# Optimization experiments

Measured on AMD Instinct MI355X. Metric: run time of the kernel, lower is better.

Reference implementation:

```python
import jax, jax.numpy as jnp
import numpy as np

N, E = 50000, 800000
IN, HID, OUT, H = 128, 32, 32, 4
NEG_SLOPE = 0.2
EPS = 1e-5


def layernorm(x, g, b):
    mu = x.mean(-1, keepdims=True)
    var = ((x - mu) ** 2).mean(-1, keepdims=True)
    return (x - mu) * jax.lax.rsqrt(var + EPS) * g + b


def gat_conv(x, src, dst, W, a_s, a_d, bias, heads, ch, concat):
    n = x.shape[0]
    h = (x @ W).reshape(n, heads, ch)               # [N,H,C]
    alpha_s = (h * a_s).sum(-1)                     # [N,H]
    alpha_d = (h * a_d).sum(-1)                     # [N,H]
    e = jax.nn.leaky_relu(alpha_s[src] + alpha_d[dst], NEG_SLOPE)  # [E,H]
    m = jax.ops.segment_max(e, dst, num_segments=n)
    m = jnp.where(jnp.isfinite(m), m, 0.0)
    ex = jnp.exp(e - m[dst])
    denom = jax.ops.segment_sum(ex, dst, num_segments=n)
    alpha = ex / (denom[dst] + 1e-16)               # [E,H]
    msg = h[src] * alpha[:, :, None]                # [E,H,C]
    out = jax.ops.segment_sum(msg, dst, num_segments=n)  # [N,H,C]
    out = out.reshape(n, heads * ch) if concat else out.mean(axis=1)
    return out + bias


def setup_inputs() -> dict:
    key = jax.random.key(0)
    ks = jax.random.split(key, 24)
    HC = HID * H
    s = 0.05
    inp = {
        "x": jax.random.normal(ks[0], (N, IN), jnp.float32),
        "edge_index": jax.random.randint(ks[1], (2, E), 0, N),
        "W1": jax.random.normal(ks[2], (IN, HC), jnp.float32) * s,
        "as1": jax.random.normal(ks[3], (H, HID), jnp.float32) * s,
        "ad1": jax.random.normal(ks[4], (H, HID), jnp.float32) * s,
        "b1": jnp.zeros((HC,), jnp.float32),
        "g1": jnp.ones((HC,), jnp.float32),
        "be1": jnp.zeros((HC,), jnp.float32),
        "W2": jax.random.normal(ks[5], (HC, HC), jnp.float32) * s,
        "as2": jax.random.normal(ks[6], (H, HID), jnp.float32) * s,
        "ad2": jax.random.normal(ks[7], (H, HID), jnp.float32) * s,
        "b2": jnp.zeros((HC,), jnp.float32),
        "g2": jnp.ones((HC,), jnp.float32),
        "be2": jnp.zeros((HC,), jnp.float32),
        "W3": jax.random.normal(ks[8], (HC, OUT * H), jnp.float32) * s,
        "as3": jax.random.normal(ks[9], (H, OUT), jnp.float32) * s,
        "ad3": jax.random.normal(ks[10], (H, OUT), jnp.float32) * s,
        "b3": jnp.zeros((OUT,), jnp.float32),
        "Wsk": jax.random.normal(ks[11], (IN, HC), jnp.float32) * s,
        "bsk": jnp.zeros((HC,), jnp.float32),
    }
    return inp


def reference(x, edge_index, W1, as1, ad1, b1, g1, be1, W2, as2, ad2, b2, g2, be2, W3, as3, ad3, b3, Wsk, bsk):
    n = x.shape[0]
    loops = jnp.arange(n, dtype=edge_index.dtype)
    src = jnp.concatenate([edge_index[0], loops])
    dst = jnp.concatenate([edge_index[1], loops])
    h = gat_conv(x, src, dst, W1, as1, ad1, b1, H, HID, True)
    h = jax.nn.elu(h)
    h = layernorm(h, g1, be1)
    h = h + (x @ Wsk + bsk)  # residual (dropout is identity in eval)
    h = gat_conv(h, src, dst, W2, as2, ad2, b2, H, HID, True)
    h = jax.nn.elu(h)
    h = layernorm(h, g2, be2)
    h = gat_conv(h, src, dst, W3, as3, ad3, b3, H, OUT, False)
    return h
```

## Files before the change

kernel.cpp:

```cpp
#include <hip/hip_runtime.h>
#include <hip/hip_bf16.h>

typedef __attribute__((ext_vector_type(8))) short short8;
typedef __attribute__((ext_vector_type(4))) float f32x4;
using bf16 = __hip_bfloat16;

#define NEG_SLOPE 0.2f
#define LN_EPS 1e-5f

__device__ __forceinline__ unsigned short f2bfu(float v) {
    bf16 t = __float2bfloat16(v);
    unsigned short s;
    __builtin_memcpy(&s, &t, 2);
    return s;
}
__device__ __forceinline__ short f2bf(float v) {
    bf16 t = __float2bfloat16(v);
    short s;
    __builtin_memcpy(&s, &t, 2);
    return s;
}
__device__ __forceinline__ unsigned packbf(float a, float b) {
    return (unsigned)f2bfu(a) | ((unsigned)f2bfu(b) << 16);
}
__device__ __forceinline__ float bflo(unsigned u) { return __uint_as_float(u << 16); }
__device__ __forceinline__ float bfhi(unsigned u) { return __uint_as_float(u & 0xffff0000u); }
__device__ __forceinline__ float bf1(unsigned short u) { return __uint_as_float(((unsigned)u) << 16); }

__global__ void detect_k(const void* __restrict__ x, int* flag,
                         int* bucketCur, int CAP) {
    int lane = threadIdx.x;
    for (int i = lane; i < 512; i += 64) bucketCur[i] = i * CAP;
    const unsigned short* u = (const unsigned short*)x;
    float m = 0.f;
    for (int i = lane; i < 8192; i += 64) {
        float v = fabsf(bf1(u[i]));
        if (!(v == v)) v = 1e30f;
        m = fmaxf(m, v);
    }
    for (int d = 1; d < 64; d <<= 1) m = fmaxf(m, __shfl_xor(m, d));
    if (lane == 0) flag[0] = (m > 1e4f) ? 1 : 0;
}

struct Ptr4 { const void* p[4]; };
struct Ptr14 { const void* p[14]; };
struct Ptr3 { const void* p[3]; };
struct Ptr6 { const void* p[6]; };
__global__ void stage_k(Ptr4 Ws, bf16* __restrict__ WT,
                        Ptr14 ptrs, bf16* __restrict__ sv,
                        Ptr3 Wv, Ptr6 av, bf16* __restrict__ vaT,
                        const int* __restrict__ flag) {
    int b = blockIdx.x;
    int f = flag[0];
    if (b < 256) {
        int gid = b * 256 + threadIdx.x;
        int m = gid >> 14;
        int idx = gid & 16383;
        int i = idx >> 7, j = idx & 127;
        const void* W = Ws.p[m];
        float v = f ? ((const float*)W)[idx]
                    : __bfloat162float(((const bf16*)W)[idx]);
        WT[m * 16384 + j * 128 + i] = __float2bfloat16(v);
    } else if (b == 256) {
        for (int k = threadIdx.x; k < 14 * 128; k += 256) {
            int t = k >> 7, i = k & 127;
            int n = (t == 12) ? 32 : 128;
            if (i < n) {
                const void* s = ptrs.p[t];
                float v = f ? ((const float*)s)[i]
                            : __bfloat162float(((const bf16*)s)[i]);
                sv[k] = __float2bfloat16(v);
            }
        }
    } else {
        int gid = (b - 257) * 256 + threadIdx.x;
        int l = gid >> 11;
        if (l >= 3) return;
        int c = (gid >> 7) & 15, k = gid & 127;
        float acc = 0.f;
        if (c < 8) {
            int hd = c & 3;
            const void* W = Wv.p[l];
            const void* a = av.p[l * 2 + (c >> 2)];
            for (int j = 0; j < 32; ++j) {
                float wv = f ? ((const float*)W)[k * 128 + hd * 32 + j]
                             : __bfloat162float(((const bf16*)W)[k * 128 + hd * 32 + j]);
                float avv = f ? ((const float*)a)[hd * 32 + j]
                              : __bfloat162float(((const bf16*)a)[hd * 32 + j]);
                acc += wv * avv;
            }
        }
        vaT[gid] = __float2bfloat16(acc);
    }
}

#define SCAT_EPB 2048
__global__ __launch_bounds__(256) void bscatter_k(const int* __restrict__ src,
                                                  const int* __restrict__ dst,
                                                  int* bucketCur,
                                                  int* __restrict__ ebuf,
                                                  int E, int NB, int CAP) {
    __shared__ int lcnt[512], lbase[512];
    int t = threadIdx.x;
    int e0 = blockIdx.x * SCAT_EPB;
    int cnt = E - e0;
    if (cnt > SCAT_EPB) cnt = SCAT_EPB;
    for (int i = t; i < NB; i += 256) lcnt[i] = 0;
    __syncthreads();
    for (int i = t; i < cnt; i += 256)
        atomicAdd(&lcnt[dst[e0 + i] >> 7], 1);
    __syncthreads();
    for (int i = t; i < NB; i += 256) {
        int c = lcnt[i];
        lbase[i] = c ? atomicAdd(&bucketCur[i], c) : 0;
        lcnt[i] = 0;
    }
    __syncthreads();
    for (int i = t; i < cnt; i += 256) {
        int d = dst[e0 + i];
        int b = d >> 7;
        int pos = lbase[b] + atomicAdd(&lcnt[b], 1);
        if (pos < (b + 1) * CAP)
            ebuf[pos] = ((d & 127) << 16) | src[e0 + i];
    }
}

__global__ __launch_bounds__(256) void build_k(const int* __restrict__ ebuf,
                                               const int* __restrict__ bucketCur,
                                               int* __restrict__ rowSE,
                                               int* __restrict__ colSrc,
                                               int N, int CAP) {
    int b = blockIdx.x, t = threadIdx.x;
    int base = b * CAP;
    int cnt = bucketCur[b] - base;
    if (cnt > CAP) cnt = CAP;
    __shared__ int nodeCnt[128], nodeCur[128], ws2[2];
    if (t < 128) nodeCnt[t] = 0;
    __syncthreads();
    for (int i = t; i < cnt; i += 256)
        atomicAdd(&nodeCnt[ebuf[base + i] >> 16], 1);
    __syncthreads();
    int v = 0, incl = 0;
    if (t < 128) {
        v = nodeCnt[t];
        incl = v;
        for (int d = 1; d < 64; d <<= 1) {
            int u = __shfl_up(incl, d);
            if ((t & 63) >= d) incl += u;
        }
        if ((t & 63) == 63) ws2[t >> 6] = incl;
    }
    __syncthreads();
    if (t < 128) {
        int excl = incl - v + ((t >= 64) ? ws2[0] : 0);
        int node = b * 128 + t;
        if (node < N) {
            rowSE[node * 2] = base + excl;
            rowSE[node * 2 + 1] = base + excl + v;
        }
        nodeCur[t] = excl;
    }
    __syncthreads();
    for (int i = t; i < cnt; i += 256) {
        int p = ebuf[base + i];
        int pos = base + atomicAdd(&nodeCur[p >> 16], 1);
        colSrc[pos] = (p & 0xffff) << 8;
    }
    int capz = CAP + ((b == (int)gridDim.x - 1) ? 32 : 0);
    for (int i = cnt + t; i < capz; i += 256)
        colSrc[base + i] = 0;
}

template <int DUAL>
__global__ __launch_bounds__(256) void gemm_k(const void* __restrict__ A,
                                              const bf16* __restrict__ WT,
                                              bf16* __restrict__ out0,
                                              bf16* __restrict__ out1,
                                              const bf16* __restrict__ bias1,
                                              const bf16* __restrict__ vaT,
                                              float* __restrict__ asN,
                                              float* __restrict__ adN,
                                              int N, const int* __restrict__ flag) {
    int wave = threadIdx.x >> 6, lane = threadIdx.x & 63;
    int lm = lane & 15, lk = lane >> 4;
    const short* Ws = (const short*)WT;
    const short* Vs = (const short*)vaT;
    bool f32m = flag && flag[0];

    short8 bw0[2][4], bw1[DUAL ? 2 : 1][DUAL ? 4 : 1];
#pragma unroll
    for (int ct = 0; ct < 2; ++ct) {
        int c = (wave * 2 + ct) * 16 + lm;
#pragma unroll
        for (int kk = 0; kk < 4; ++kk)
            bw0[ct][kk] = *(const short8*)(Ws + (size_t)c * 128 + kk * 32 + lk * 8);
    }
    if (DUAL) {
#pragma unroll
        for (int ct = 0; ct < 2; ++ct) {
            int c = (wave * 2 + ct) * 16 + lm;
#pragma unroll
            for (int kk = 0; kk < 4; ++kk)
                bw1[ct][kk] = *(const short8*)(Ws + 16384 + (size_t)c * 128 + kk * 32 + lk * 8);
        }
    }
    short8 va8[4];
    if (wave == 0) {
#pragma unroll
        for (int kk = 0; kk < 4; ++kk)
            va8[kk] = *(const short8*)(Vs + (size_t)lm * 128 + kk * 32 + lk * 8);
    }
    float bv[2][4];
    if (DUAL) {
#pragma unroll
        for (int ct = 0; ct < 2; ++ct) {
            int c0 = (wave * 2 + ct) * 16 + lk * 4;
#pragma unroll
            for (int i = 0; i < 4; ++i)
                bv[ct][i] = __bfloat162float(bias1[c0 + i]);
        }
    }

    int stride = gridDim.x * 32;
    for (int rowBase = blockIdx.x * 32; rowBase < N; rowBase += stride) {
        short8 af[2][4];
#pragma unroll
        for (int rt = 0; rt < 2; ++rt) {
            int r = rowBase + rt * 16 + lm;
            if (r >= N) r = N - 1;
            if (f32m) {
#pragma unroll
                for (int kk = 0; kk < 4; ++kk) {
                    const float* Af = (const float*)A + (size_t)r * 128 + kk * 32 + lk * 8;
                    float4 q0 = *(const float4*)(Af);
                    float4 q1 = *(const float4*)(Af + 4);
                    short8 v;
                    v[0] = f2bf(q0.x); v[1] = f2bf(q0.y); v[2] = f2bf(q0.z); v[3] = f2bf(q0.w);
                    v[4] = f2bf(q1.x); v[5] = f2bf(q1.y); v[6] = f2bf(q1.z); v[7] = f2bf(q1.w);
                    af[rt][kk] = v;
                }
            } else {
#pragma unroll
                for (int kk = 0; kk < 4; ++kk)
                    af[rt][kk] = *(const short8*)((const short*)A + (size_t)r * 128 + kk * 32 + lk * 8);
            }
        }

        f32x4 acc0[2][2];
        f32x4 acc1[DUAL ? 2 : 1][DUAL ? 2 : 1];
#pragma unroll
        for (int ct = 0; ct < 2; ++ct)
#pragma unroll
            for (int rt = 0; rt < 2; ++rt) acc0[ct][rt] = (f32x4){0.f, 0.f, 0.f, 0.f};
        if (DUAL) {
#pragma unroll
            for (int ct = 0; ct < 2; ++ct)
#pragma unroll
                for (int rt = 0; rt < 2; ++rt) acc1[ct][rt] = (f32x4){0.f, 0.f, 0.f, 0.f};
        }

#pragma unroll
        for (int rt = 0; rt < 2; ++rt) {
#pragma unroll
            for (int kk = 0; kk < 4; ++kk) {
                acc0[0][rt] = __builtin_amdgcn_mfma_f32_16x16x32_bf16(bw0[0][kk], af[rt][kk], acc0[0][rt], 0, 0, 0);
                acc0[1][rt] = __builtin_amdgcn_mfma_f32_16x16x32_bf16(bw0[1][kk], af[rt][kk], acc0[1][rt], 0, 0, 0);
                if (DUAL) {
                    acc1[0][rt] = __builtin_amdgcn_mfma_f32_16x16x32_bf16(bw1[0][kk], af[rt][kk], acc1[0][rt], 0, 0, 0);
                    acc1[1][rt] = __builtin_amdgcn_mfma_f32_16x16x32_bf16(bw1[1][kk], af[rt][kk], acc1[1][rt], 0, 0, 0);
                }
            }
        }

#pragma unroll
        for (int ct = 0; ct < 2; ++ct) {
            int c0 = (wave * 2 + ct) * 16 + lk * 4;
#pragma unroll
            for (int rt = 0; rt < 2; ++rt) {
                int r = rowBase + rt * 16 + lm;
                if (r < N) {
                    uint2 pk;
                    pk.x = packbf(acc0[ct][rt][0], acc0[ct][rt][1]);
                    pk.y = packbf(acc0[ct][rt][2], acc0[ct][rt][3]);
                    *(uint2*)((unsigned short*)out0 + (size_t)r * 128 + c0) = pk;
                }
            }
        }
        if (DUAL) {
#pragma unroll
            for (int ct = 0; ct < 2; ++ct) {
                int c0 = (wave * 2 + ct) * 16 + lk * 4;
#pragma unroll
                for (int rt = 0; rt < 2; ++rt) {
                    int r = rowBase + rt * 16 + lm;
                    if (r < N) {
                        uint2 pk;
                        pk.x = packbf(acc1[ct][rt][0] + bv[ct][0], acc1[ct][rt][1] + bv[ct][1]);
                        pk.y = packbf(acc1[ct][rt][2] + bv[ct][2], acc1[ct][rt][3] + bv[ct][3]);
                        *(uint2*)((unsigned short*)out1 + (size_t)r * 128 + c0) = pk;
                    }
                }
            }
        }

        if (wave == 0) {
            f32x4 accA[2];
#pragma unroll
            for (int rt = 0; rt < 2; ++rt) accA[rt] = (f32x4){0.f, 0.f, 0.f, 0.f};
#pragma unroll
            for (int rt = 0; rt < 2; ++rt)
#pragma unroll
                for (int kk = 0; kk < 4; ++kk)
                    accA[rt] = __builtin_amdgcn_mfma_f32_16x16x32_bf16(va8[kk], af[rt][kk], accA[rt], 0, 0, 0);
            if (lk < 2) {
                float* dp = lk ? adN : asN;
#pragma unroll
                for (int rt = 0; rt < 2; ++rt) {
                    int r = rowBase + rt * 16 + lm;
                    if (r < N) *(f32x4*)(dp + (size_t)r * 4) = accA[rt];
                }
            }
        }
    }
}

template <int MODE>
__global__ __launch_bounds__(256) void agg_k(const bf16* __restrict__ h,
                                             const float* __restrict__ asN,
                                             const float* __restrict__ adN,
                                             const int* __restrict__ rowSE,
                                             const int* __restrict__ colSrc,
                                             const bf16* __restrict__ bvec,
                                             const bf16* __restrict__ g,
                                             const bf16* __restrict__ be,
                                             void* outv, int N,
                                             const int* __restrict__ flag) {
    int wv = threadIdx.x >> 6, lane = threadIdx.x & 63;
    int grp = lane >> 4, t = lane & 15;
    int hd = t >> 2;
    const char* hbase = (const char*)h + t * 16;
    const char* abase = (const char*)asN + hd * 4;
    int f = (MODE == 3 && flag) ? flag[0] : 0;
    int nstride = gridDim.x * 4;

    for (int n = blockIdx.x * 4 + wv; n < N; n += nstride) {
        int2 se = ((const int2*)rowSE)[n];
        int st = se.x, en = se.y;
        if (en < st) en = st;

        float adn = adN[(size_t)n * 4 + hd];
        float asn_self = asN[(size_t)n * 4 + hd];
        unsigned hs = *(const unsigned*)((const char*)h + (size_t)n * 256 + t * 16 + grp * 4);

        float a[8];
#pragma unroll
        for (int k = 0; k < 8; ++k) a[k] = 0.f;
        float den = 0.f;

        int j = st + grp;
        int o0 = (j      < en) ? colSrc[j]      : 0;
        int o1 = (j + 4  < en) ? colSrc[j + 4]  : 0;
        int o2 = (j + 8  < en) ? colSrc[j + 8]  : 0;
        int o3 = (j + 12 < en) ? colSrc[j + 12] : 0;
        float av0 = *(const float*)(abase + (o0 >> 4));
        uint4 hq0 = *(const uint4*)(hbase + o0);
        float av1 = *(const float*)(abase + (o1 >> 4));
        uint4 hq1 = *(const uint4*)(hbase + o1);
        float av2 = *(const float*)(abase + (o2 >> 4));
        uint4 hq2 = *(const uint4*)(hbase + o2);
        for (; j < en; j += 4) {
            int o4 = (j + 16 < en) ? colSrc[j + 16] : 0;
            float av3 = *(const float*)(abase + (o3 >> 4));
            uint4 hq3 = *(const uint4*)(hbase + o3);
            float e = av0 + adn;
            float w = __expf(fmaxf(e, NEG_SLOPE * e));
            den += w;
            a[0] += w * bflo(hq0.x); a[1] += w * bfhi(hq0.x);
            a[2] += w * bflo(hq0.y); a[3] += w * bfhi(hq0.y);
            a[4] += w * bflo(hq0.z); a[5] += w * bfhi(hq0.z);
            a[6] += w * bflo(hq0.w); a[7] += w * bfhi(hq0.w);
            o3 = o4;
            av0 = av1; hq0 = hq1;
            av1 = av2; hq1 = hq2;
            av2 = av3; hq2 = hq3;
        }

#pragma unroll
        for (int k = 0; k < 8; ++k) {
            a[k] += __shfl_xor(a[k], 16);
            a[k] += __shfl_xor(a[k], 32);
        }
        den += __shfl_xor(den, 16);
        den += __shfl_xor(den, 32);

        float es = asn_self + adn;
        float wsf = __expf(fmaxf(es, NEG_SLOPE * es));
        den += wsf;

        float s0 = (grp & 1) ? a[2] : a[0];
        float s1 = (grp & 1) ? a[3] : a[1];
        float s2 = (grp & 1) ? a[6] : a[4];
        float s3 = (grp & 1) ? a[7] : a[5];
        float p0 = (grp & 2) ? s2 : s0;
        float p1 = (grp & 2) ? s3 : s1;

        p0 += wsf * bflo(hs);
        p1 += wsf * bfhi(hs);

        float inv = 1.f / (den + 1e-16f);
        float y0 = p0 * inv, y1 = p1 * inv;

        if (MODE == 3) {
            y0 += __shfl_xor(y0, 4); y0 += __shfl_xor(y0, 8); y0 *= 0.25f;
            y1 += __shfl_xor(y1, 4); y1 += __shfl_xor(y1, 8); y1 *= 0.25f;
            if (t < 4) {
                int oc = t * 8 + grp * 2;
                unsigned bp = *(const unsigned*)((const char*)bvec + oc * 2);
                float v0 = y0 + bflo(bp), v1 = y1 + bfhi(bp);
                if (f) {
                    *(float2*)((float*)outv + (size_t)n * 32 + oc) = make_float2(v0, v1);
                } else {
                    ((unsigned*)outv)[(size_t)n * 16 + (oc >> 1)] = packbf(v0, v1);
                }
            }
        } else {
            unsigned short* out = (unsigned short*)outv;
            int boff = t * 16 + grp * 4;
            unsigned bp = *(const unsigned*)((const char*)bvec + boff);
            y0 += bflo(bp); y1 += bfhi(bp);
            y0 = y0 > 0.f ? y0 : (__expf(y0) - 1.f);
            y1 = y1 > 0.f ? y1 : (__expf(y1) - 1.f);
            float s = y0 + y1, q = y0 * y0 + y1 * y1;
#pragma unroll
            for (int d = 1; d < 64; d <<= 1) {
                s += __shfl_xor(s, d);
                q += __shfl_xor(q, d);
            }
            float mu = s * (1.f / 128.f);
            float var = q * (1.f / 128.f) - mu * mu;
            var = fmaxf(var, 0.f);
            float rs = rsqrtf(var + LN_EPS);
            unsigned gp = *(const unsigned*)((const char*)g + boff);
            unsigned ep = *(const unsigned*)((const char*)be + boff);
            float z0 = (y0 - mu) * rs * bflo(gp) + bflo(ep);
            float z1 = (y1 - mu) * rs * bfhi(gp) + bfhi(ep);
            char* op = (char*)out + (size_t)n * 256 + boff;
            if (MODE == 1) {
                unsigned sk = *(const unsigned*)op;
                z0 += bflo(sk); z1 += bfhi(sk);
            }
            *(unsigned*)op = packbf(z0, z1);
        }
    }
}

extern "C" void kernel_launch(void* const* d_in, const int* in_sizes, int n_in,
                              void* d_out, int out_size, void* d_ws, size_t ws_size,
                              hipStream_t stream) {
    const void* x  = d_in[0];
    const int*  ei = (const int*)d_in[1];

    int N = in_sizes[0] / 128;
    int E = in_sizes[1] / 2;
    const int* srcI = ei;
    const int* dstI = ei + E;

    int NB = (N + 127) >> 7;
    int CAP = (E / NB + 1024 + 511) & ~511;

    char* w = (char*)d_ws;
    size_t o = 0;
    auto carve = [&](size_t bytes) {
        void* p = w + o;
        o += (bytes + 255) & ~(size_t)255;
        return p;
    };
    int*  dtFlag = (int*)carve(256);
    bf16* WTall = (bf16*)carve(4 * 16384 * 2);
    bf16* sv   = (bf16*)carve(14 * 128 * 2);
    bf16* vaT  = (bf16*)carve(3 * 16 * 128 * 2);
    bf16* hB   = (bf16*)carve((size_t)N * 128 * 2);
    bf16* xB   = (bf16*)carve((size_t)N * 128 * 2);
    float* asN = (float*)carve((size_t)N * 4 * 4);
    float* adN = (float*)carve((size_t)N * 4 * 4);
    int* rowSE = (int*)carve((size_t)N * 2 * 4);
    int* colSrc= (int*)carve((size_t)NB * CAP * 4 + 128);
    int* ebuf  = (int*)carve((size_t)NB * CAP * 4);
    int* bucketCur = (int*)carve(512 * 4);

    detect_k<<<1, 64, 0, stream>>>(x, dtFlag, bucketCur, CAP);

    Ptr4 wp;
    wp.p[0] = d_in[2];  wp.p[1] = d_in[18];
    wp.p[2] = d_in[8];  wp.p[3] = d_in[14];
    Ptr14 ptrs;
    ptrs.p[0] = d_in[3];  ptrs.p[1] = d_in[4];  ptrs.p[2] = d_in[5];
    ptrs.p[3] = d_in[6];  ptrs.p[4] = d_in[7];
    ptrs.p[5] = d_in[9];  ptrs.p[6] = d_in[10]; ptrs.p[7] = d_in[11];
    ptrs.p[8] = d_in[12]; ptrs.p[9] = d_in[13];
    ptrs.p[10] = d_in[15]; ptrs.p[11] = d_in[16]; ptrs.p[12] = d_in[17];
    ptrs.p[13] = d_in[19];
    Ptr3 wv3;
    wv3.p[0] = d_in[2]; wv3.p[1] = d_in[8]; wv3.p[2] = d_in[14];
    Ptr6 av6;
    av6.p[0] = d_in[3];  av6.p[1] = d_in[4];
    av6.p[2] = d_in[9];  av6.p[3] = d_in[10];
    av6.p[4] = d_in[15]; av6.p[5] = d_in[16];

    stage_k<<<281, 256, 0, stream>>>(wp, WTall, ptrs, sv, wv3, av6, vaT, dtFlag);

    bscatter_k<<<(E + SCAT_EPB - 1) / SCAT_EPB, 256, 0, stream>>>(srcI, dstI,
                                                                 bucketCur, ebuf, E, NB, CAP);
    build_k<<<NB, 256, 0, stream>>>(ebuf, bucketCur, rowSE, colSrc, N, CAP);

    int gb = (N + 63) / 64;
    int nQuads = (N + 3) / 4;
    int aggGrid = nQuads < 2048 ? nQuads : 2048;

    gemm_k<1><<<gb, 256, 0, stream>>>(x, WTall, hB, xB, sv + 13 * 128,
                                      vaT, asN, adN, N, dtFlag);
    agg_k<1><<<aggGrid, 256, 0, stream>>>(hB, asN, adN, rowSE, colSrc,
                                          sv + 2 * 128, sv + 3 * 128, sv + 4 * 128,
                                          xB, N, dtFlag);

    gemm_k<0><<<gb, 256, 0, stream>>>(xB, WTall + 2 * 16384, hB, nullptr, nullptr,
                                      vaT + 2048, asN, adN, N, nullptr);
    agg_k<2><<<aggGrid, 256, 0, stream>>>(hB, asN, adN, rowSE, colSrc,
                                          sv + 7 * 128, sv + 8 * 128, sv + 9 * 128,
                                          xB, N, dtFlag);

    gemm_k<0><<<gb, 256, 0, stream>>>(xB, WTall + 3 * 16384, hB, nullptr, nullptr,
                                      vaT + 4096, asN, adN, N, nullptr);
    agg_k<3><<<aggGrid, 256, 0, stream>>>(hB, asN, adN, rowSE, colSrc,
                                          sv + 12 * 128, nullptr, nullptr,
                                          d_out, N, dtFlag);
}
```

Measured before the change: 330.8 us.

## Fuse dtype detection into staging and bucket scatter into first GEMM launch

Removes the separate detect kernel: every stage_k block recomputes the dtype flag from x, and block 256 also initializes the bucket cursors. The edge bucket-scatter is folded into the first dual GEMM launch as extra blocks, so scatter and GEMM run concurrently in one dispatch. SCAT_EPB is doubled, the colSrc zero-padding tail in build_k is dropped, and gemm_k is simplified to its non-dual bf16 form. This cuts launch count and serialization, but every staging block now repeats the flag scan, and the removed padding may matter if agg reads past the valid entries.

```diff
diff --git a/kernel.cpp b/kernel.cpp
--- a/kernel.cpp
+++ b/kernel.cpp
@@ -7,6 +7,7 @@
 
 #define NEG_SLOPE 0.2f
 #define LN_EPS 1e-5f
+#define SCAT_EPB 4096
 
 __device__ __forceinline__ unsigned short f2bfu(float v) {
     bf16 t = __float2bfloat16(v);
@@ -27,31 +28,37 @@
 __device__ __forceinline__ float bfhi(unsigned u) { return __uint_as_float(u & 0xffff0000u); }
 __device__ __forceinline__ float bf1(unsigned short u) { return __uint_as_float(((unsigned)u) << 16); }
 
-__global__ void detect_k(const void* __restrict__ x, int* flag,
-                         int* bucketCur, int CAP) {
-    int lane = threadIdx.x;
-    for (int i = lane; i < 512; i += 64) bucketCur[i] = i * CAP;
-    const unsigned short* u = (const unsigned short*)x;
+__device__ __forceinline__ int computeFlag(const void* x) {
+    const uint4* u4 = (const uint4*)x;
+    int lane = threadIdx.x & 63;
     float m = 0.f;
-    for (int i = lane; i < 8192; i += 64) {
-        float v = fabsf(bf1(u[i]));
-        if (!(v == v)) v = 1e30f;
-        m = fmaxf(m, v);
+    for (int i = lane; i < 1024; i += 64) {
+        uint4 q = u4[i];
+        unsigned vv[4] = {q.x, q.y, q.z, q.w};
+#pragma unroll
+        for (int k = 0; k < 4; ++k) {
+            float a = fabsf(bflo(vv[k]));
+            float b = fabsf(bfhi(vv[k]));
+            m = fmaxf(m, (a == a) ? a : 1e30f);
+            m = fmaxf(m, (b == b) ? b : 1e30f);
+        }
     }
     for (int d = 1; d < 64; d <<= 1) m = fmaxf(m, __shfl_xor(m, d));
-    if (lane == 0) flag[0] = (m > 1e4f) ? 1 : 0;
+    return (m > 1e4f) ? 1 : 0;
 }
 
 struct Ptr4 { const void* p[4]; };
 struct Ptr14 { const void* p[14]; };
 struct Ptr3 { const void* p[3]; };
 struct Ptr6 { const void* p[6]; };
-__global__ void stage_k(Ptr4 Ws, bf16* __restrict__ WT,
+__global__ void stage_k(const void* __restrict__ x,
+                        Ptr4 Ws, bf16* __restrict__ WT,
                         Ptr14 ptrs, bf16* __restrict__ sv,
                         Ptr3 Wv, Ptr6 av, bf16* __restrict__ vaT,
-                        const int* __restrict__ flag) {
+                        int* __restrict__ dtFlag, int* __restrict__ bucketCur,
+                        int CAP) {
     int b = blockIdx.x;
-    int f = flag[0];
+    int f = computeFlag(x);
     if (b < 256) {
         int gid = b * 256 + threadIdx.x;
         int m = gid >> 14;
@@ -62,6 +69,8 @@
                     : __bfloat162float(((const bf16*)W)[idx]);
         WT[m * 16384 + j * 128 + i] = __float2bfloat16(v);
     } else if (b == 256) {
+        for (int i = threadIdx.x; i < 512; i += 256) bucketCur[i] = i * CAP;
+        if (threadIdx.x == 0) dtFlag[0] = f;
         for (int k = threadIdx.x; k < 14 * 128; k += 256) {
             int t = k >> 7, i = k & 127;
             int n = (t == 12) ? 32 : 128;
@@ -94,34 +103,149 @@
     }
 }
 
-#define SCAT_EPB 2048
-__global__ __launch_bounds__(256) void bscatter_k(const int* __restrict__ src,
-                                                  const int* __restrict__ dst,
-                                                  int* bucketCur,
-                                                  int* __restrict__ ebuf,
-                                                  int E, int NB, int CAP) {
+__global__ __launch_bounds__(256) void mega1_k(
+        const void* __restrict__ A, const bf16* __restrict__ WT,
+        bf16* __restrict__ out0, bf16* __restrict__ out1,
+        const bf16* __restrict__ bias1, const bf16* __restrict__ vaT,
+        float* __restrict__ asN, float* __restrict__ adN,
+        int N, const int* __restrict__ flag, int gb,
+        const int* __restrict__ src, const int* __restrict__ dst,
+        int* bucketCur, int* __restrict__ ebuf, int E, int NB, int CAP) {
     __shared__ int lcnt[512], lbase[512];
-    int t = threadIdx.x;
-    int e0 = blockIdx.x * SCAT_EPB;
-    int cnt = E - e0;
-    if (cnt > SCAT_EPB) cnt = SCAT_EPB;
-    for (int i = t; i < NB; i += 256) lcnt[i] = 0;
-    __syncthreads();
-    for (int i = t; i < cnt; i += 256)
-        atomicAdd(&lcnt[dst[e0 + i] >> 7], 1);
-    __syncthreads();
-    for (int i = t; i < NB; i += 256) {
-        int c = lcnt[i];
-        lbase[i] = c ? atomicAdd(&bucketCur[i], c) : 0;
-        lcnt[i] = 0;
-    }
-    __syncthreads();
-    for (int i = t; i < cnt; i += 256) {
-        int d = dst[e0 + i];
-        int b = d >> 7;
-        int pos = lbase[b] + atomicAdd(&lcnt[b], 1);
-        if (pos < (b + 1) * CAP)
-            ebuf[pos] = ((d & 127) << 16) | src[e0 + i];
+    if ((int)blockIdx.x >= gb) {
+        int t = threadIdx.x;
+        int e0 = ((int)blockIdx.x - gb) * SCAT_EPB;
+        int cnt = E - e0;
+        if (cnt > SCAT_EPB) cnt = SCAT_EPB;
+        for (int i = t; i < NB; i += 256) lcnt[i] = 0;
+        __syncthreads();
+        for (int i = t; i < cnt; i += 256)
+            atomicAdd(&lcnt[dst[e0 + i] >> 7], 1);
+        __syncthreads();
+        for (int i = t; i < NB; i += 256) {
+            int c = lcnt[i];
+            lbase[i] = c ? atomicAdd(&bucketCur[i], c) : 0;
+            lcnt[i] = 0;
+        }
+        __syncthreads();
+        for (int i = t; i < cnt; i += 256) {
+            int d = dst[e0 + i];
+            int b = d >> 7;
+            int pos = lbase[b] + atomicAdd(&lcnt[b], 1);
+            if (pos < (b + 1) * CAP)
+                ebuf[pos] = ((d & 127) << 16) | src[e0 + i];
+        }
+        return;
+    }
+    int wave = threadIdx.x >> 6, lane = threadIdx.x & 63;
+    int lm = lane & 15, lk = lane >> 4;
+    const short* Ws = (const short*)WT;
+    const short* Vs = (const short*)vaT;
+    bool f32m = flag[0] != 0;
+
+    short8 bw0[2][4], bw1[2][4];
+#pragma unroll
+    for (int ct = 0; ct < 2; ++ct) {
+        int c = (wave * 2 + ct) * 16 + lm;
+#pragma unroll
+        for (int kk = 0; kk < 4; ++kk) {
+            bw0[ct][kk] = *(const short8*)(Ws + (size_t)c * 128 + kk * 32 + lk * 8);
+            bw1[ct][kk] = *(const short8*)(Ws + 16384 + (size_t)c * 128 + kk * 32 + lk * 8);
+        }
+    }
+    short8 va8[4];
+    if (wave == 0) {
+#pragma unroll
+        for (int kk = 0; kk < 4; ++kk)
+            va8[kk] = *(const short8*)(Vs + (size_t)lm * 128 + kk * 32 + lk * 8);
+    }
+    float bv[2][4];
+#pragma unroll
+    for (int ct = 0; ct < 2; ++ct) {
+        int c0 = (wave * 2 + ct) * 16 + lk * 4;
+#pragma unroll
+        for (int i = 0; i < 4; ++i)
+            bv[ct][i] = __bfloat162float(bias1[c0 + i]);
+    }
+
+    int stride = gb * 32;
+    for (int rowBase = blockIdx.x * 32; rowBase < N; rowBase += stride) {
+        short8 af[2][4];
+#pragma unroll
+        for (int rt = 0; rt < 2; ++rt) {
+            int r = rowBase + rt * 16 + lm;
+            if (r >= N) r = N - 1;
+            if (f32m) {
+#pragma unroll
+                for (int kk = 0; kk < 4; ++kk) {
+                    const float* Af = (const float*)A + (size_t)r * 128 + kk * 32 + lk * 8;
+                    float4 q0 = *(const float4*)(Af);
+                    float4 q1 = *(const float4*)(Af + 4);
+                    short8 v;
+                    v[0] = f2bf(q0.x); v[1] = f2bf(q0.y); v[2] = f2bf(q0.z); v[3] = f2bf(q0.w);
+                    v[4] = f2bf(q1.x); v[5] = f2bf(q1.y); v[6] = f2bf(q1.z); v[7] = f2bf(q1.w);
+                    af[rt][kk] = v;
+                }
+            } else {
+#pragma unroll
+                for (int kk = 0; kk < 4; ++kk)
+                    af[rt][kk] = *(const short8*)((const short*)A + (size_t)r * 128 + kk * 32 + lk * 8);
+            }
+        }
+
+        f32x4 acc0[2][2], acc1[2][2];
+#pragma unroll
+        for (int ct = 0; ct < 2; ++ct)
+#pragma unroll
+            for (int rt = 0; rt < 2; ++rt) {
+                acc0[ct][rt] = (f32x4){0.f, 0.f, 0.f, 0.f};
+                acc1[ct][rt] = (f32x4){0.f, 0.f, 0.f, 0.f};
+            }
+#pragma unroll
+        for (int rt = 0; rt < 2; ++rt) {
+#pragma unroll
+            for (int kk = 0; kk < 4; ++kk) {
+                acc0[0][rt] = __builtin_amdgcn_mfma_f32_16x16x32_bf16(bw0[0][kk], af[rt][kk], acc0[0][rt], 0, 0, 0);
+                acc0[1][rt] = __builtin_amdgcn_mfma_f32_16x16x32_bf16(bw0[1][kk], af[rt][kk], acc0[1][rt], 0, 0, 0);
+                acc1[0][rt] = __builtin_amdgcn_mfma_f32_16x16x32_bf16(bw1[0][kk], af[rt][kk], acc1[0][rt], 0, 0, 0);
+                acc1[1][rt] = __builtin_amdgcn_mfma_f32_16x16x32_bf16(bw1[1][kk], af[rt][kk], acc1[1][rt], 0, 0, 0);
+            }
+        }
+#pragma unroll
+        for (int ct = 0; ct < 2; ++ct) {
+            int c0 = (wave * 2 + ct) * 16 + lk * 4;
+#pragma unroll
+            for (int rt = 0; rt < 2; ++rt) {
+                int r = rowBase + rt * 16 + lm;
+                if (r < N) {
+                    uint2 pk0, pk1;
+                    pk0.x = packbf(acc0[ct][rt][0], acc0[ct][rt][1]);
+                    pk0.y = packbf(acc0[ct][rt][2], acc0[ct][rt][3]);
+                    pk1.x = packbf(acc1[ct][rt][0] + bv[ct][0], acc1[ct][rt][1] + bv[ct][1]);
+                    pk1.y = packbf(acc1[ct][rt][2] + bv[ct][2], acc1[ct][rt][3] + bv[ct][3]);
+                    *(uint2*)((unsigned short*)out0 + (size_t)r * 128 + c0) = pk0;
+                    *(uint2*)((unsigned short*)out1 + (size_t)r * 128 + c0) = pk1;
+                }
+            }
+        }
+        if (wave == 0) {
+            f32x4 accA[2];
+#pragma unroll
+            for (int rt = 0; rt < 2; ++rt) accA[rt] = (f32x4){0.f, 0.f, 0.f, 0.f};
+#pragma unroll
+            for (int rt = 0; rt < 2; ++rt)
+#pragma unroll
+                for (int kk = 0; kk < 4; ++kk)
+                    accA[rt] = __builtin_amdgcn_mfma_f32_16x16x32_bf16(va8[kk], af[rt][kk], accA[rt], 0, 0, 0);
+            if (lk < 2) {
+                float* dp = lk ? adN : asN;
+#pragma unroll
+                for (int rt = 0; rt < 2; ++rt) {
+                    int r = rowBase + rt * 16 + lm;
+                    if (r < N) *(f32x4*)(dp + (size_t)r * 4) = accA[rt];
+                }
+            }
+        }
     }
 }
 
@@ -166,28 +290,21 @@
         int pos = base + atomicAdd(&nodeCur[p >> 16], 1);
         colSrc[pos] = (p & 0xffff) << 8;
     }
-    int capz = CAP + ((b == (int)gridDim.x - 1) ? 32 : 0);
-    for (int i = cnt + t; i < capz; i += 256)
-        colSrc[base + i] = 0;
-}
-
-template <int DUAL>
+}
+
 __global__ __launch_bounds__(256) void gemm_k(const void* __restrict__ A,
                                               const bf16* __restrict__ WT,
                                               bf16* __restrict__ out0,
-                                              bf16* __restrict__ out1,
-                                              const bf16* __restrict__ bias1,
                                               const bf16* __restrict__ vaT,
                                               float* __restrict__ asN,
                                               float* __restrict__ adN,
-                                              int N, const int* __restrict__ flag) {
+                                              int N) {
     int wave = threadIdx.x >> 6, lane = threadIdx.x & 63;
     int lm = lane & 15, lk = lane >> 4;
     const short* Ws = (const short*)WT;
     const short* Vs = (const short*)vaT;
-    bool f32m = flag && flag[0];
-
-    short8 bw0[2][4], bw1[DUAL ? 2 : 1][DUAL ? 4 : 1];
+
+    short8 bw0[2][4];
 #pragma unroll
     for (int ct = 0; ct < 2; ++ct) {
         int c = (wave * 2 + ct) * 16 + lm;
@@ -195,30 +312,11 @@
         for (int kk = 0; kk < 4; ++kk)
             bw0[ct][kk] = *(const short8*)(Ws + (size_t)c * 128 + kk * 32 + lk * 8);
     }
-    if (DUAL) {
-#pragma unroll
-        for (int ct = 0; ct < 2; ++ct) {
-            int c = (wave * 2 + ct) * 16 + lm;
-#pragma unroll
-            for (int kk = 0; kk < 4; ++kk)
-                bw1[ct][kk] = *(const short8*)(Ws + 16384 + (size_t)c * 128 + kk * 32 + lk * 8);
-        }
-    }
     short8 va8[4];
     if (wave == 0) {
 #pragma unroll
         for (int kk = 0; kk < 4; ++kk)
             va8[kk] = *(const short8*)(Vs + (size_t)lm * 128 + kk * 32 + lk * 8);
-    }
-    float bv[2][4];
-    if (DUAL) {
-#pragma unroll
-        for (int ct = 0; ct < 2; ++ct) {
-            int c0 = (wave * 2 + ct) * 16 + lk * 4;
-#pragma unroll
-            for (int i = 0; i < 4; ++i)
-                bv[ct][i] = __bfloat162float(bias1[c0 + i]);
-        }
     }
 
     int stride = gridDim.x * 32;
@@ -228,50 +326,24 @@
         for (int rt = 0; rt < 2; ++rt) {
             int r = rowBase + rt * 16 + lm;
             if (r >= N) r = N - 1;
-            if (f32m) {
-#pragma unroll
-                for (int kk = 0; kk < 4; ++kk) {
-                    const float* Af = (const float*)A + (size_t)r * 128 + kk * 32 + lk * 8;
-                    float4 q0 = *(const float4*)(Af);
-                    float4 q1 = *(const float4*)(Af + 4);
-                    short8 v;
-                    v[0] = f2bf(q0.x); v[1] = f2bf(q0.y); v[2] = f2bf(q0.z); v[3] = f2bf(q0.w);
-                    v[4] = f2bf(q1.x); v[5] = f2bf(q1.y); v[6] = f2bf(q1.z); v[7] = f2bf(q1.w);
-                    af[rt][kk] = v;
-                }
-            } else {
-#pragma unroll
-                for (int kk = 0; kk < 4; ++kk)
-                    af[rt][kk] = *(const short8*)((const short*)A + (size_t)r * 128 + kk * 32 + lk * 8);
-            }
+#pragma unroll
+            for (int kk = 0; kk < 4; ++kk)
+                af[rt][kk] = *(const short8*)((const short*)A + (size_t)r * 128 + kk * 32 + lk * 8);
         }
 
         f32x4 acc0[2][2];
-        f32x4 acc1[DUAL ? 2 : 1][DUAL ? 2 : 1];
 #pragma unroll
         for (int ct = 0; ct < 2; ++ct)
 #pragma unroll
             for (int rt = 0; rt < 2; ++rt) acc0[ct][rt] = (f32x4){0.f, 0.f, 0.f, 0.f};
-        if (DUAL) {
-#pragma unroll
-            for (int ct = 0; ct < 2; ++ct)
-#pragma unroll
-                for (int rt = 0; rt < 2; ++rt) acc1[ct][rt] = (f32x4){0.f, 0.f, 0.f, 0.f};
-        }
-
 #pragma unroll
         for (int rt = 0; rt < 2; ++rt) {
 #pragma unroll
             for (int kk = 0; kk < 4; ++kk) {
                 acc0[0][rt] = __builtin_amdgcn_mfma_f32_16x16x32_bf16(bw0[0][kk], af[rt][kk], acc0[0][rt], 0, 0, 0);
                 acc0[1][rt] = __builtin_amdgcn_mfma_f32_16x16x32_bf16(bw0[1][kk], af[rt][kk], acc0[1][rt], 0, 0, 0);
-                if (DUAL) {
-                    acc1[0][rt] = __builtin_amdgcn_mfma_f32_16x16x32_bf16(bw1[0][kk], af[rt][kk], acc1[0][rt], 0, 0, 0);
-                    acc1[1][rt] = __builtin_amdgcn_mfma_f32_16x16x32_bf16(bw1[1][kk], af[rt][kk], acc1[1][rt], 0, 0, 0);
-                }
-            }
-        }
-
+            }
+        }
 #pragma unroll
         for (int ct = 0; ct < 2; ++ct) {
             int c0 = (wave * 2 + ct) * 16 + lk * 4;
@@ -286,23 +358,6 @@
                 }
             }
         }
-        if (DUAL) {
-#pragma unroll
-            for (int ct = 0; ct < 2; ++ct) {
-                int c0 = (wave * 2 + ct) * 16 + lk * 4;
-#pragma unroll
-                for (int rt = 0; rt < 2; ++rt) {
-                    int r = rowBase + rt * 16 + lm;
-                    if (r < N) {
-                        uint2 pk;
-                        pk.x = packbf(acc1[ct][rt][0] + bv[ct][0], acc1[ct][rt][1] + bv[ct][1]);
-                        pk.y = packbf(acc1[ct][rt][2] + bv[ct][2], acc1[ct][rt][3] + bv[ct][3]);
-                        *(uint2*)((unsigned short*)out1 + (size_t)r * 128 + c0) = pk;
-                    }
-                }
-            }
-        }
-
         if (wave == 0) {
             f32x4 accA[2];
 #pragma unroll
@@ -488,8 +543,6 @@
     int* ebuf  = (int*)carve((size_t)NB * CAP * 4);
     int* bucketCur = (int*)carve(512 * 4);
 
-    detect_k<<<1, 64, 0, stream>>>(x, dtFlag, bucketCur, CAP);
-
     Ptr4 wp;
     wp.p[0] = d_in[2];  wp.p[1] = d_in[18];
     wp.p[2] = d_in[8];  wp.p[3] = d_in[14];
@@ -507,30 +560,32 @@
     av6.p[2] = d_in[9];  av6.p[3] = d_in[10];
     av6.p[4] = d_in[15]; av6.p[5] = d_in[16];
 
-    stage_k<<<281, 256, 0, stream>>>(wp, WTall, ptrs, sv, wv3, av6, vaT, dtFlag);
-
-    bscatter_k<<<(E + SCAT_EPB - 1) / SCAT_EPB, 256, 0, stream>>>(srcI, dstI,
-                                                                 bucketCur, ebuf, E, NB, CAP);
-    build_k<<<NB, 256, 0, stream>>>(ebuf, bucketCur, rowSE, colSrc, N, CAP);
+    stage_k<<<281, 256, 0, stream>>>(x, wp, WTall, ptrs, sv, wv3, av6, vaT,
+                                     dtFlag, bucketCur, CAP);
 
     int gb = (N + 63) / 64;
+    int scatB = (E + SCAT_EPB - 1) / SCAT_EPB;
     int nQuads = (N + 3) / 4;
     int aggGrid = nQuads < 2048 ? nQuads : 2048;
 
-    gemm_k<1><<<gb, 256, 0, stream>>>(x, WTall, hB, xB, sv + 13 * 128,
-                                      vaT, asN, adN, N, dtFlag);
+    mega1_k<<<gb + scatB, 256, 0, stream>>>(x, WTall, hB, xB, sv + 13 * 128,
+                                            vaT, asN, adN, N, dtFlag, gb,
+                                            srcI, dstI, bucketCur, ebuf, E, NB, CAP);
+
+    build_k<<<NB, 256, 0, stream>>>(ebuf, bucketCur, rowSE, colSrc, N, CAP);
+
     agg_k<1><<<aggGrid, 256, 0, stream>>>(hB, asN, adN, rowSE, colSrc,
                                           sv + 2 * 128, sv + 3 * 128, sv + 4 * 128,
                                           xB, N, dtFlag);
 
-    gemm_k<0><<<gb, 256, 0, stream>>>(xB, WTall + 2 * 16384, hB, nullptr, nullptr,
-                                      vaT + 2048, asN, adN, N, nullptr);
+    gemm_k<<<gb, 256, 0, stream>>>(xB, WTall + 2 * 16384, hB,
+                                   vaT + 2048, asN, adN, N);
     agg_k<2><<<aggGrid, 256, 0, stream>>>(hB, asN, adN, rowSE, colSrc,
                                           sv + 7 * 128, sv + 8 * 128, sv + 9 * 128,
                                           xB, N, dtFlag);
 
-    gemm_k<0><<<gb, 256, 0, stream>>>(xB, WTall + 3 * 16384, hB, nullptr, nullptr,
-                                      vaT + 4096, asN, adN, N, nullptr);
+    gemm_k<<<gb, 256, 0, stream>>>(xB, WTall + 3 * 16384, hB,
+                                   vaT + 4096, asN, adN, N);
     agg_k<3><<<aggGrid, 256, 0, stream>>>(hB, asN, adN, rowSE, colSrc,
                                           sv + 12 * 128, nullptr, nullptr,
                                           d_out, N, dtFlag);
```

After: 308.0 us. 1.07x faster.
